# Kernel optimization log

Measured on AMD Instinct MI355X. Metric: run time of the kernel, lower is better.

Reference implementation:

```python
import jax, jax.numpy as jnp
import numpy as np
from jax import lax

C_IN = 256
C_OUT = 256
KS = 3


def _conv(x, w, b):
    # x: [B,C,H,W], w: [O,I,kh,kw] -> NCHW 'SAME' conv, stride 1
    y = lax.conv_general_dilated(x, w, window_strides=(1, 1), padding='SAME',
                                 dimension_numbers=('NCHW', 'OIHW', 'NCHW'))
    return y + b[None, :, None, None]


def setup_inputs() -> dict:
    key = jax.random.key(0)
    ks = jax.random.split(key, 7)
    B, H, W = 2, 64, 64
    fan = C_IN * KS * KS
    lim = float(np.sqrt(6.0 / (fan + C_OUT * KS * KS)))  # xavier uniform
    return {
        'x': jax.random.normal(ks[0], (B, C_IN, H, W), jnp.float32),
        'ref_x': jax.random.normal(ks[1], (B, C_IN, H, W), jnp.float32),
        'conv1_w': jax.random.uniform(ks[2], (C_OUT, C_IN, KS, KS), jnp.float32, -lim, lim),
        'conv1_b': jnp.zeros((C_OUT,), jnp.float32),
        'conv2_w': jax.random.uniform(ks[3], (C_OUT, C_IN, KS, KS), jnp.float32, -lim, lim),
        'conv2_b': jnp.zeros((C_OUT,), jnp.float32),
        'gamma': jnp.array([0.5], jnp.float32),
    }


def reference(x, ref_x, conv1_w, conv1_b, conv2_w, conv2_b, gamma):
    B, Cin, H, W = x.shape
    HW = H * W
    x_f = jax.nn.relu(_conv(x, conv1_w, conv1_b)).reshape(B, C_OUT, HW)        # [B,C,HW]
    r_f = jax.nn.relu(_conv(ref_x, conv1_w, conv1_b))                          # [B,C,H,W]
    r_f = r_f.transpose(0, 2, 3, 1).reshape(B, HW, C_OUT)                      # [B,HW,C]
    corr = jnp.einsum('bnc,bcm->bnm', r_f, x_f)                                # [B,HW,HW]
    corr = jax.nn.softmax(corr, axis=1)                                        # softmax over ref positions
    ref_c2 = jax.nn.relu(_conv(x, conv2_w, conv2_b)).reshape(B, C_OUT, HW)     # [B,C,HW]
    A = jnp.einsum('bcn,bnm->bcm', ref_c2, corr).reshape(x.shape)              # [B,C,H,W]
    return A * gamma[0] + x
```

## Files before the change

kernel.cpp:

```cpp
#include <hip/hip_runtime.h>
#include <hip/hip_bf16.h>

#define B_ 2
#define C_ 256
#define H_ 64
#define W_ 64
#define N_ 4096

typedef short bf16x8 __attribute__((ext_vector_type(8)));
typedef _Float16 f16x8 __attribute__((ext_vector_type(8)));
typedef float f32x4 __attribute__((ext_vector_type(4)));
typedef float f32x16 __attribute__((ext_vector_type(16)));

static __device__ __forceinline__ unsigned short f2bf(float f) {
    union { float f; unsigned u; } uf; uf.f = f;
    unsigned r = uf.u + 0x7fffu + ((uf.u >> 16) & 1u);
    return (unsigned short)(r >> 16);
}
static __device__ __forceinline__ unsigned short f2h_u(float f) {
    union { _Float16 h; unsigned short u; } c; c.h = (_Float16)f; return c.u;
}

static __device__ __forceinline__ void gload16(const void* g, void* l) {
    __builtin_amdgcn_global_load_lds(
        (const __attribute__((address_space(1))) unsigned int*)g,
        (__attribute__((address_space(3))) unsigned int*)l, 16, 0, 0);
}

__global__ __launch_bounds__(256) void cvt_x_k(const float* __restrict__ x,
                                               const float* __restrict__ ref_x,
                                               unsigned short* __restrict__ xtx,
                                               unsigned short* __restrict__ xtr)
{
    __shared__ unsigned short t[64][72];
    const int pt = blockIdx.x, ct = blockIdx.y;
    const int which = blockIdx.z >> 1, b = blockIdx.z & 1;
    const float* in = which ? ref_x : x;
    unsigned short* out = which ? xtr : xtx;
    const int a = threadIdx.x & 63, r = threadIdx.x >> 6;
    #pragma unroll
    for (int i = 0; i < 16; ++i) {
        int c = i * 4 + r;
        t[c][a] = f2h_u(in[((size_t)(b * C_ + ct * 64 + c) << 12) + pt * 64 + a]);
    }
    __syncthreads();
    #pragma unroll
    for (int i = 0; i < 16; ++i) {
        int p = i * 4 + r;
        out[((size_t)(b * N_ + pt * 64 + p) << 8) + ct * 64 + a] = t[a][p];
    }
}

__global__ __launch_bounds__(256) void cvt_w_k(const float* __restrict__ w1,
                                               const float* __restrict__ w2,
                                               unsigned short* __restrict__ wh1,
                                               unsigned short* __restrict__ wh2)
{
    int g = blockIdx.x;
    const float* w = (g < 2304) ? w1 : w2;
    unsigned short* wh = (g < 2304) ? wh1 : wh2;
    int i = (g % 2304) * 256 + threadIdx.x;
    int ci = i & 255, co = (i >> 8) & 255, tap = i >> 16;
    wh[i] = f2h_u(w[((size_t)(co * 256 + ci)) * 9 + tap]);
}

__global__ __launch_bounds__(256) void conv_mfma_k(
    const unsigned short* __restrict__ xtx, const unsigned short* __restrict__ xtr,
    const unsigned short* __restrict__ w1h, const unsigned short* __restrict__ w2h,
    const float* __restrict__ b1, const float* __restrict__ b2,
    unsigned short* __restrict__ f1x, unsigned short* __restrict__ f1r,
    unsigned short* __restrict__ f2)
{
    __shared__ unsigned short As[4 * 576 * 8];
    __shared__ unsigned short Bs[4 * 66 * 32];
    const int tid = threadIdx.x;
    const int pt  = blockIdx.x;
    const int cot = blockIdx.y;
    const int cid = blockIdx.z >> 1;
    const int b   = blockIdx.z & 1;

    const unsigned short* xt = (cid == 1) ? xtr : xtx;
    const unsigned short* wt = (cid == 2) ? w2h : w1h;
    const float* bias = (cid == 2) ? b2 : b1;
    unsigned short* out = (cid == 0) ? f1x : (cid == 1) ? f1r : f2;
    const int trans = (cid != 2);

    const int lane = tid & 63, wid = tid >> 6;
    const int wco = wid >> 1, wpos = wid & 1;
    const int rl = lane & 15, q = lane >> 4;
    const int r0 = pt * 2;

    f32x4 acc[2][4];
    #pragma unroll
    for (int mi = 0; mi < 2; ++mi)
        #pragma unroll
        for (int ni = 0; ni < 4; ++ni)
            #pragma unroll
            for (int e = 0; e < 4; ++e) acc[mi][ni][e] = 0.f;

    for (int k0 = 0; k0 < C_; k0 += 32) {
        #pragma unroll
        for (int tap = 0; tap < 9; ++tap) {
            gload16(wt + ((size_t)(tap * C_ + cot * 64 + lane) << 8) + k0 + wid * 8,
                    &As[(wid * 576 + tap * 64 + lane) * 8]);
        }
        #pragma unroll
        for (int j = 0; j < 5; ++j) {
            int it = tid + j * 256;
            if (it < 1056) {
                int col = it >> 4, sub = it & 15;
                int row = sub >> 2, qb = sub & 3;
                int h = r0 + row - 1, c = col - 1;
                float4 v; v.x = 0.f; v.y = 0.f; v.z = 0.f; v.w = 0.f;
                if (h >= 0 && h < 64 && c >= 0 && c < 64)
                    v = *(const float4*)(xt + ((size_t)(b * N_ + h * 64 + c) << 8) + k0 + qb * 8);
                int chunk = qb ^ ((col >> 1) & 3);
                *(float4*)&Bs[(row * 66 + col) * 32 + chunk * 8] = v;
            }
        }
        __syncthreads();

        #pragma unroll
        for (int tap = 0; tap < 9; ++tap) {
            const int kh = tap / 3, kw = tap % 3;
            f16x8 a0 = *(const f16x8*)&As[(q * 576 + tap * 64 + wco * 32 + rl) * 8];
            f16x8 a1 = *(const f16x8*)&As[(q * 576 + tap * 64 + wco * 32 + 16 + rl) * 8];
            const int chunkB = q ^ (((rl + kw) >> 1) & 3);
            const int rowB = (wpos + kh) * 66;
            #pragma unroll
            for (int ni = 0; ni < 4; ++ni) {
                int colB = ni * 16 + rl + kw;
                f16x8 bf = *(const f16x8*)&Bs[(rowB + colB) * 32 + chunkB * 8];
                acc[0][ni] = __builtin_amdgcn_mfma_f32_16x16x32_f16(a0, bf, acc[0][ni], 0, 0, 0);
                acc[1][ni] = __builtin_amdgcn_mfma_f32_16x16x32_f16(a1, bf, acc[1][ni], 0, 0, 0);
            }
        }
        __syncthreads();
    }

    #pragma unroll
    for (int mi = 0; mi < 2; ++mi) {
        const int co = cot * 64 + wco * 32 + mi * 16 + q * 4;
        float bs[4];
        #pragma unroll
        for (int rr = 0; rr < 4; ++rr) bs[rr] = bias[co + rr];
        #pragma unroll
        for (int ni = 0; ni < 4; ++ni) {
            const int pos = pt * 128 + wpos * 64 + ni * 16 + rl;
            if (trans) {
                unsigned short pk[4];
                #pragma unroll
                for (int rr = 0; rr < 4; ++rr)
                    pk[rr] = f2bf(fmaxf(acc[mi][ni][rr] + bs[rr], 0.f));
                uint2 u;
                u.x = (unsigned)pk[0] | ((unsigned)pk[1] << 16);
                u.y = (unsigned)pk[2] | ((unsigned)pk[3] << 16);
                *(uint2*)&out[((size_t)(b * N_ + pos) << 8) + co] = u;
            } else {
                #pragma unroll
                for (int rr = 0; rr < 4; ++rr)
                    out[((size_t)(b * C_ + co + rr) << 12) + pos] =
                        f2bf(fmaxf(acc[mi][ni][rr] + bs[rr], 0.f));
            }
        }
    }
}

__global__ __launch_bounds__(256, 2) void flash_k(
    const unsigned short* __restrict__ f1x,
    const unsigned short* __restrict__ f1r,
    const unsigned short* __restrict__ f2,
    float* __restrict__ part,
    float* __restrict__ stats)
{
    __shared__ unsigned short Ks[64 * 264];
    __shared__ unsigned short Vs[256 * 72];
    const int tid = threadIdx.x;
    const int mt = blockIdx.x, s = blockIdx.y, b = blockIdx.z;
    const int m0 = mt * 32;
    const int lane = tid & 63, wid = tid >> 6;
    const int wn = wid & 1, wc2 = wid >> 1;
    const int rl = lane & 31, l5 = lane >> 5;
    const int c0w = wc2 * 128;
    const int nw = wn * 32;

    bf16x8 Qf[16];
    #pragma unroll
    for (int st = 0; st < 16; ++st)
        Qf[st] = *(const bf16x8*)&f1x[(((size_t)b * N_ + m0 + rl) << 8) + st * 16 + l5 * 8];

    f32x16 O[4];
    #pragma unroll
    for (int cf = 0; cf < 4; ++cf)
        #pragma unroll
        for (int e = 0; e < 16; ++e) O[cf][e] = 0.f;
    float m_run = -1e30f, l_run = 0.f;

    const int nbase = s * 2048;
    for (int r = 0; r < 32; ++r) {
        const int n0 = nbase + r * 64;
        #pragma unroll
        for (int j = 0; j < 8; ++j) {
            int it = tid + j * 256;
            int n = it >> 5, cq = it & 31;
            *(float4*)&Ks[n * 264 + cq * 8] =
                *(const float4*)&f1r[(((size_t)b * N_ + n0 + n) << 8) + cq * 8];
        }
        #pragma unroll
        for (int j = 0; j < 8; ++j) {
            int it = tid + j * 256;
            int c = it >> 3, nq = it & 7;
            *(float4*)&Vs[c * 72 + nq * 8] =
                *(const float4*)&f2[(((size_t)b * C_ + c) << 12) + n0 + nq * 8];
        }
        __syncthreads();

        f32x16 S;
        #pragma unroll
        for (int e = 0; e < 16; ++e) S[e] = 0.f;
        #pragma unroll
        for (int st = 0; st < 16; ++st) {
            bf16x8 Kf = *(const bf16x8*)&Ks[(nw + rl) * 264 + st * 16 + l5 * 8];
            S = __builtin_amdgcn_mfma_f32_32x32x16_bf16(Kf, Qf[st], S, 0, 0, 0);
        }

        float mx = S[0];
        #pragma unroll
        for (int e = 1; e < 16; ++e) mx = fmaxf(mx, S[e]);
        mx = fmaxf(mx, __shfl_xor(mx, 32));
        float m_new = fmaxf(m_run, mx);
        float sc = __expf(m_run - m_new);
        float p[16]; float lsum = 0.f;
        #pragma unroll
        for (int e = 0; e < 16; ++e) { p[e] = __expf(S[e] - m_new); lsum += p[e]; }
        l_run = l_run * sc + lsum;
        m_run = m_new;
        #pragma unroll
        for (int cf = 0; cf < 4; ++cf)
            #pragma unroll
            for (int e = 0; e < 16; ++e) O[cf][e] *= sc;

        unsigned pk_[8], xk[8];
        #pragma unroll
        for (int g = 0; g < 8; ++g)
            pk_[g] = (unsigned)f2bf(p[2 * g]) | ((unsigned)f2bf(p[2 * g + 1]) << 16);
        #pragma unroll
        for (int g = 0; g < 8; ++g) xk[g] = (unsigned)__shfl_xor((int)pk_[g], 32);
        union { unsigned d[4]; bf16x8 v; } P0, P1;
        P0.d[0] = l5 ? xk[2] : pk_[0];
        P0.d[1] = l5 ? xk[3] : pk_[1];
        P0.d[2] = l5 ? pk_[2] : xk[0];
        P0.d[3] = l5 ? pk_[3] : xk[1];
        P1.d[0] = l5 ? xk[6] : pk_[4];
        P1.d[1] = l5 ? xk[7] : pk_[5];
        P1.d[2] = l5 ? pk_[6] : xk[4];
        P1.d[3] = l5 ? pk_[7] : xk[5];

        #pragma unroll
        for (int cf = 0; cf < 4; ++cf) {
            const int vrow = (c0w + cf * 32 + rl) * 72;
            bf16x8 Vf0 = *(const bf16x8*)&Vs[vrow + nw + l5 * 8];
            O[cf] = __builtin_amdgcn_mfma_f32_32x32x16_bf16(Vf0, P0.v, O[cf], 0, 0, 0);
            bf16x8 Vf1 = *(const bf16x8*)&Vs[vrow + nw + 16 + l5 * 8];
            O[cf] = __builtin_amdgcn_mfma_f32_32x32x16_bf16(Vf1, P1.v, O[cf], 0, 0, 0);
        }
        __syncthreads();
    }

    float l_tot = l_run + __shfl_xor(l_run, 32);
    const int se = s * 2 + wn;
    float* pb = part + (size_t)se * ((size_t)B_ * C_ * N_);
    #pragma unroll
    for (int cf = 0; cf < 4; ++cf)
        #pragma unroll
        for (int e = 0; e < 16; ++e) {
            int c = c0w + cf * 32 + (e & 3) + 8 * (e >> 2) + 4 * l5;
            pb[(((size_t)b * C_ + c) << 12) + m0 + rl] = O[cf][e];
        }
    if (wc2 == 0 && l5 == 0) {
        float2 st; st.x = m_run; st.y = l_tot;
        ((float2*)stats)[(((size_t)(se * 2 + b)) << 12) + m0 + rl] = st;
    }
}

__global__ __launch_bounds__(256) void combine_k(
    const float* __restrict__ part, const float* __restrict__ stats,
    const float* __restrict__ x, const float* __restrict__ gamma,
    float* __restrict__ out)
{
    const float g = gamma[0];
    size_t i = (size_t)blockIdx.x * 256 + threadIdx.x;
    size_t idx = i << 2;
    const int m = (int)(idx & 4095);
    const int b = (int)(idx >> 20);
    const size_t PS = (size_t)B_ * C_ * N_;

    float ms[4][4], ls[4][4];
    #pragma unroll
    for (int se = 0; se < 4; ++se) {
        const float2* sp = (const float2*)stats + (((size_t)(se * 2 + b)) << 12) + m;
        #pragma unroll
        for (int j = 0; j < 4; ++j) { float2 v = sp[j]; ms[se][j] = v.x; ls[se][j] = v.y; }
    }
    float w[4][4], den[4] = {0.f, 0.f, 0.f, 0.f};
    #pragma unroll
    for (int j = 0; j < 4; ++j) {
        float M = fmaxf(fmaxf(ms[0][j], ms[1][j]), fmaxf(ms[2][j], ms[3][j]));
        #pragma unroll
        for (int se = 0; se < 4; ++se) {
            w[se][j] = __expf(ms[se][j] - M);
            den[j] += w[se][j] * ls[se][j];
        }
    }
    float num[4] = {0.f, 0.f, 0.f, 0.f};
    #pragma unroll
    for (int se = 0; se < 4; ++se) {
        float4 p = *(const float4*)&part[se * PS + idx];
        num[0] += w[se][0] * p.x; num[1] += w[se][1] * p.y;
        num[2] += w[se][2] * p.z; num[3] += w[se][3] * p.w;
    }
    float4 xv = ((const float4*)x)[i];
    float4 o;
    o.x = g * num[0] / den[0] + xv.x;
    o.y = g * num[1] / den[1] + xv.y;
    o.z = g * num[2] / den[2] + xv.z;
    o.w = g * num[3] / den[3] + xv.w;
    ((float4*)out)[i] = o;
}

extern "C" void kernel_launch(void* const* d_in, const int* in_sizes, int n_in,
                              void* d_out, int out_size, void* d_ws, size_t ws_size,
                              hipStream_t stream) {
    const float* x     = (const float*)d_in[0];
    const float* ref_x = (const float*)d_in[1];
    const float* w1    = (const float*)d_in[2];
    const float* b1    = (const float*)d_in[3];
    const float* w2    = (const float*)d_in[4];
    const float* b2    = (const float*)d_in[5];
    const float* gamma = (const float*)d_in[6];
    float* out = (float*)d_out;

    char* ws = (char*)d_ws;
    size_t off = 0;
    auto nxt = [&](size_t bytes) {
        char* p = ws + off;
        off += (bytes + 255) & ~(size_t)255;
        return p;
    };
    unsigned short* f1x = (unsigned short*)nxt((size_t)B_ * N_ * C_ * 2);
    unsigned short* f1r = (unsigned short*)nxt((size_t)B_ * N_ * C_ * 2);
    unsigned short* f2  = (unsigned short*)nxt((size_t)B_ * N_ * C_ * 2);
    unsigned short* xtx = (unsigned short*)nxt((size_t)B_ * N_ * C_ * 2);
    unsigned short* xtr = (unsigned short*)nxt((size_t)B_ * N_ * C_ * 2);
    unsigned short* w1h = (unsigned short*)nxt((size_t)9 * C_ * C_ * 2);
    unsigned short* w2h = (unsigned short*)nxt((size_t)9 * C_ * C_ * 2);
    float* part  = (float*)nxt((size_t)4 * B_ * C_ * N_ * 4);
    float* stats = (float*)nxt((size_t)4 * B_ * N_ * 8);

    cvt_x_k<<<dim3(64, 4, 4), 256, 0, stream>>>(x, ref_x, xtx, xtr);
    cvt_w_k<<<4608, 256, 0, stream>>>(w1, w2, w1h, w2h);

    conv_mfma_k<<<dim3(32, 4, 6), 256, 0, stream>>>(xtx, xtr, w1h, w2h, b1, b2,
                                                    f1x, f1r, f2);

    flash_k<<<dim3(128, 2, 2), 256, 0, stream>>>(f1x, f1r, f2, part, stats);
    combine_k<<<2048, 256, 0, stream>>>(part, stats, x, gamma, out);
}
```

Baseline: 150.5 us.

## Prefetch next K/V tile into registers and use lazy softmax rescaling

The flash attention loop now loads the next K and V tiles from global memory into registers while the current tile is being computed, then writes them to LDS after the second barrier. This hides global load latency behind the MFMA work. The change also splits the QK accumulation into two independent MFMA chains, skips rescaling the output when the running max grows by no more than a threshold, and uses the hardware packed bf16 convert instruction. The cost is higher register pressure from 16 float4 prefetch registers under launch bounds of 2 blocks per CU. The skipped rescale also allows exponentials up to e^8 in bf16 P.

```diff
diff --git a/kernel.cpp b/kernel.cpp
--- a/kernel.cpp
+++ b/kernel.cpp
@@ -19,6 +19,11 @@
 }
 static __device__ __forceinline__ unsigned short f2h_u(float f) {
     union { _Float16 h; unsigned short u; } c; c.h = (_Float16)f; return c.u;
+}
+static __device__ __forceinline__ unsigned cvtpk_bf16(float lo, float hi) {
+    unsigned r;
+    asm("v_cvt_pk_bf16_f32 %0, %1, %2" : "=v"(r) : "v"(lo), "v"(hi));
+    return r;
 }
 
 static __device__ __forceinline__ void gload16(const void* g, void* l) {
@@ -184,6 +189,9 @@
     const int c0w = wc2 * 128;
     const int nw = wn * 32;
 
+    const int kn = tid >> 5, kq = tid & 31;
+    const int vc = tid >> 3, vq = tid & 7;
+
     bf16x8 Qf[16];
     #pragma unroll
     for (int st = 0; st < 16; ++st)
@@ -197,53 +205,79 @@
     float m_run = -1e30f, l_run = 0.f;
 
     const int nbase = s * 2048;
+
+    float4 kreg[8], vreg[8];
+    #pragma unroll
+    for (int j = 0; j < 8; ++j) {
+        kreg[j] = *(const float4*)&f1r[(((size_t)b * N_ + nbase + kn + j * 8) << 8) + kq * 8];
+        vreg[j] = *(const float4*)&f2[(((size_t)b * C_ + vc + j * 32) << 12) + nbase + vq * 8];
+    }
+    #pragma unroll
+    for (int j = 0; j < 8; ++j) {
+        *(float4*)&Ks[(kn + j * 8) * 264 + kq * 8] = kreg[j];
+        *(float4*)&Vs[(vc + j * 32) * 72 + vq * 8] = vreg[j];
+    }
+
     for (int r = 0; r < 32; ++r) {
-        const int n0 = nbase + r * 64;
-        #pragma unroll
-        for (int j = 0; j < 8; ++j) {
-            int it = tid + j * 256;
-            int n = it >> 5, cq = it & 31;
-            *(float4*)&Ks[n * 264 + cq * 8] =
-                *(const float4*)&f1r[(((size_t)b * N_ + n0 + n) << 8) + cq * 8];
-        }
-        #pragma unroll
-        for (int j = 0; j < 8; ++j) {
-            int it = tid + j * 256;
-            int c = it >> 3, nq = it & 7;
-            *(float4*)&Vs[c * 72 + nq * 8] =
-                *(const float4*)&f2[(((size_t)b * C_ + c) << 12) + n0 + nq * 8];
-        }
         __syncthreads();
 
-        f32x16 S;
-        #pragma unroll
-        for (int e = 0; e < 16; ++e) S[e] = 0.f;
-        #pragma unroll
-        for (int st = 0; st < 16; ++st) {
-            bf16x8 Kf = *(const bf16x8*)&Ks[(nw + rl) * 264 + st * 16 + l5 * 8];
-            S = __builtin_amdgcn_mfma_f32_32x32x16_bf16(Kf, Qf[st], S, 0, 0, 0);
-        }
-
-        float mx = S[0];
-        #pragma unroll
-        for (int e = 1; e < 16; ++e) mx = fmaxf(mx, S[e]);
+        if (r < 31) {
+            const int n0 = nbase + (r + 1) * 64;
+            #pragma unroll
+            for (int j = 0; j < 8; ++j) {
+                kreg[j] = *(const float4*)&f1r[(((size_t)b * N_ + n0 + kn + j * 8) << 8) + kq * 8];
+                vreg[j] = *(const float4*)&f2[(((size_t)b * C_ + vc + j * 32) << 12) + n0 + vq * 8];
+            }
+        }
+
+        f32x16 Sa, Sb;
+        #pragma unroll
+        for (int e = 0; e < 16; ++e) { Sa[e] = 0.f; Sb[e] = 0.f; }
+        const int krow = (nw + rl) * 264 + l5 * 8;
+        #pragma unroll
+        for (int st = 0; st < 16; st += 2) {
+            bf16x8 Kf0 = *(const bf16x8*)&Ks[krow + st * 16];
+            bf16x8 Kf1 = *(const bf16x8*)&Ks[krow + st * 16 + 16];
+            Sa = __builtin_amdgcn_mfma_f32_32x32x16_bf16(Kf0, Qf[st], Sa, 0, 0, 0);
+            Sb = __builtin_amdgcn_mfma_f32_32x32x16_bf16(Kf1, Qf[st + 1], Sb, 0, 0, 0);
+        }
+        float S[16];
+        #pragma unroll
+        for (int e = 0; e < 16; ++e) S[e] = Sa[e] + Sb[e];
+
+        float t8[8];
+        #pragma unroll
+        for (int e = 0; e < 8; ++e) t8[e] = fmaxf(S[e], S[e + 8]);
+        float t4a = fmaxf(t8[0], t8[4]), t4b = fmaxf(t8[1], t8[5]);
+        float t4c = fmaxf(t8[2], t8[6]), t4d = fmaxf(t8[3], t8[7]);
+        float mx = fmaxf(fmaxf(t4a, t4b), fmaxf(t4c, t4d));
         mx = fmaxf(mx, __shfl_xor(mx, 32));
-        float m_new = fmaxf(m_run, mx);
-        float sc = __expf(m_run - m_new);
-        float p[16]; float lsum = 0.f;
-        #pragma unroll
-        for (int e = 0; e < 16; ++e) { p[e] = __expf(S[e] - m_new); lsum += p[e]; }
-        l_run = l_run * sc + lsum;
-        m_run = m_new;
-        #pragma unroll
-        for (int cf = 0; cf < 4; ++cf)
+
+        if (!__all(mx <= m_run + 8.f)) {
+            float m_new = fmaxf(m_run, mx);
+            float sc = __expf(m_run - m_new);
+            l_run *= sc;
             #pragma unroll
-            for (int e = 0; e < 16; ++e) O[cf][e] *= sc;
+            for (int cf = 0; cf < 4; ++cf)
+                #pragma unroll
+                for (int e = 0; e < 16; ++e) O[cf][e] *= sc;
+            m_run = m_new;
+        }
+
+        float p[16];
+        float ls0 = 0.f, ls1 = 0.f, ls2 = 0.f, ls3 = 0.f;
+        #pragma unroll
+        for (int e = 0; e < 16; e += 4) {
+            p[e]     = __expf(S[e]     - m_run); ls0 += p[e];
+            p[e + 1] = __expf(S[e + 1] - m_run); ls1 += p[e + 1];
+            p[e + 2] = __expf(S[e + 2] - m_run); ls2 += p[e + 2];
+            p[e + 3] = __expf(S[e + 3] - m_run); ls3 += p[e + 3];
+        }
+        l_run += (ls0 + ls1) + (ls2 + ls3);
 
         unsigned pk_[8], xk[8];
         #pragma unroll
-        for (int g = 0; g < 8; ++g)
-            pk_[g] = (unsigned)f2bf(p[2 * g]) | ((unsigned)f2bf(p[2 * g + 1]) << 16);
+        for (int g = 0; g < 8; ++g) pk_[g] = cvtpk_bf16(p[2 * g], p[2 * g + 1]);
         #pragma unroll
         for (int g = 0; g < 8; ++g) xk[g] = (unsigned)__shfl_xor((int)pk_[g], 32);
         union { unsigned d[4]; bf16x8 v; } P0, P1;
@@ -265,6 +299,14 @@
             O[cf] = __builtin_amdgcn_mfma_f32_32x32x16_bf16(Vf1, P1.v, O[cf], 0, 0, 0);
         }
         __syncthreads();
+
+        if (r < 31) {
+            #pragma unroll
+            for (int j = 0; j < 8; ++j) {
+                *(float4*)&Ks[(kn + j * 8) * 264 + kq * 8] = kreg[j];
+                *(float4*)&Vs[(vc + j * 32) * 72 + vq * 8] = vreg[j];
+            }
+        }
     }
 
     float l_tot = l_run + __shfl_xor(l_run, 32);
```

New measurement: 439.9 us. +192.4%, slower.
